# Kernel tuning notes

Hardware: AMD Instinct MI355X
Metric: run time of the kernel (lower is better)

The kernel has to match this reference:

```python
import jax, jax.numpy as jnp
import numpy as np

B, N, F_IN, F_OUT = 8, 2048, 128, 64
ALPHA = 0.2  # LeakyReLU negative slope
NEG_BIG = -9e15


def setup_inputs() -> dict:
    key = jax.random.key(0)
    k1, k2, k3, k4 = jax.random.split(key, 4)
    x = jax.random.normal(k1, (B, N, F_IN), dtype=jnp.float32)
    adj = jax.random.randint(k2, (B, N, N), 0, 2, dtype=jnp.int32)
    # xavier-uniform-ish init scale for faithfulness (gain=1.414)
    w_lim = 1.414 * np.sqrt(6.0 / (F_IN + F_OUT))
    a_lim = 1.414 * np.sqrt(6.0 / (2 * F_OUT + 1))
    weight = jax.random.uniform(k3, (F_IN, F_OUT), minval=-w_lim, maxval=w_lim, dtype=jnp.float32)
    weight2 = jax.random.uniform(k4, (2 * F_OUT, 1), minval=-a_lim, maxval=a_lim, dtype=jnp.float32)
    return {"x": x, "adj": adj, "weight": weight, "weight2": weight2}


def reference(x, adj, weight, weight2):
    # Linear projection: [B, N, F_out]
    wh = jnp.einsum("bnf,fo->bno", x, weight)
    # Additive GAT decomposition of concat-score:
    # e_ij = leakyrelu(a1 . Wh_i + a2 . Wh_j)  == original concat @ weight2
    a1 = weight2[:F_OUT, 0]   # [F_out]
    a2 = weight2[F_OUT:, 0]   # [F_out]
    s1 = wh @ a1              # [B, N]
    s2 = wh @ a2              # [B, N]
    e = s1[:, :, None] + s2[:, None, :]          # [B, N, N]
    e = jnp.where(e > 0, e, ALPHA * e)            # LeakyReLU
    e = jnp.where(adj > 0, e, NEG_BIG)            # mask non-edges
    attention = jax.nn.softmax(e, axis=2)         # [B, N, N]
    # dropout is identity in eval mode (training=False)
    out = jnp.einsum("bij,bjo->bio", attention, wh)  # [B, N, F_out]
    return jax.nn.elu(out)
```

## Files before the change

### kernel.cpp

```cpp
#include <hip/hip_runtime.h>
#include <cstdint>
#include <cstddef>

#define B_    8
#define N_    2048
#define FIN   128
#define FOUT  64
#define ALPHA 0.2f
#define NEG_BIG -9.0e15f

typedef __attribute__((ext_vector_type(8))) _Float16 half8;
typedef __attribute__((ext_vector_type(4))) float float4v;

__global__ __launch_bounds__(256, 4) void k1_wh(
    const float* __restrict__ x, const float* __restrict__ W,
    const float* __restrict__ w2, _Float16* __restrict__ whT,
    float* __restrict__ s1, float* __restrict__ s2)
{
    int t = threadIdx.x, lane = t & 63, w = t >> 6;
    float a1 = w2[lane], a2 = w2[FOUT + lane];
    int rowBase = blockIdx.x * 32 + w * 8;
    for (int rr = 0; rr < 8; ++rr) {
        int row = __builtin_amdgcn_readfirstlane(rowBase + rr);
        const float* xr = x + (size_t)row * FIN;
        float acc = 0.f;
        #pragma unroll
        for (int k = 0; k < FIN; ++k)
            acc = fmaf(xr[k], W[k * FOUT + lane], acc);
        int b = row >> 11, j = row & (N_ - 1);
        whT[((size_t)b * FOUT + lane) * N_ + j] = (_Float16)acc;
        float p1 = acc * a1, p2 = acc * a2;
        #pragma unroll
        for (int m = 32; m >= 1; m >>= 1) {
            p1 += __shfl_xor(p1, m);
            p2 += __shfl_xor(p2, m);
        }
        if (lane == 0) { s1[row] = p1; s2[row] = p2; }
    }
}

__global__ __launch_bounds__(256, 4) void k2_attn(
    const int* __restrict__ adj, const _Float16* __restrict__ whT,
    const float* __restrict__ s1, const float* __restrict__ s2,
    float* __restrict__ out)
{
    __shared__ float accL[4][16][68];
    __shared__ float lL[4][16];
    __shared__ float smaxL[4];

    int t = threadIdx.x, lane = t & 63, w = t >> 6;
    int r0 = blockIdx.x * 16;
    int b = r0 >> 11, i0 = r0 & (N_ - 1);

    const float4* s2v = (const float4*)(s2 + (size_t)b * N_);
    float4 ua = s2v[t], ub = s2v[t + 256];
    float vm = fmaxf(fmaxf(fmaxf(ua.x, ua.y), fmaxf(ua.z, ua.w)),
                     fmaxf(fmaxf(ub.x, ub.y), fmaxf(ub.z, ub.w)));
    #pragma unroll
    for (int m = 32; m >= 1; m >>= 1) vm = fmaxf(vm, __shfl_xor(vm, m));
    if (lane == 0) smaxL[w] = vm;
    __syncthreads();
    float s2max = fmaxf(fmaxf(smaxL[0], smaxL[1]), fmaxf(smaxL[2], smaxL[3]));

    int l15 = lane & 15, quad = lane >> 4;
    float s1i = s1[(size_t)b * N_ + i0 + l15];
    float mh  = s1i + s2max;
    mh = fmaxf(mh, ALPHA * mh);
    float negmh = -mh;

    float4v acc0 = {0,0,0,0}, acc1 = {0,0,0,0}, acc2 = {0,0,0,0}, acc3 = {0,0,0,0};
    float lsum = 0.f;

    const int jseg = w * 512;
    const int*      adjp = adj + ((size_t)b * N_ + i0 + l15) * N_ + jseg + quad * 8;
    const float*    s2p  = s2  + (size_t)b * N_ + jseg + quad * 8;
    const _Float16* wp   = whT + (size_t)b * FOUT * N_ + (size_t)l15 * N_ + jseg + quad * 8;

    for (int c = 0; c < 16; ++c) {
        int4   aj0 = *(const int4*)(adjp);
        int4   aj1 = *(const int4*)(adjp + 4);
        float4 sa  = *(const float4*)(s2p);
        float4 sb  = *(const float4*)(s2p + 4);
        adjp += 32; s2p += 32;

        int   aa[8] = {aj0.x, aj0.y, aj0.z, aj0.w, aj1.x, aj1.y, aj1.z, aj1.w};
        float ss[8] = {sa.x, sa.y, sa.z, sa.w, sb.x, sb.y, sb.z, sb.w};
        half8 af;
        #pragma unroll
        for (int e = 0; e < 8; ++e) {
            float v = s1i + ss[e];
            v = fmaxf(v, ALPHA * v);
            v = (aa[e] > 0) ? v : NEG_BIG;
            float tt = fmaxf(v + negmh, -76.f);
            float p = __expf(tt);
            lsum += p;
            af[e] = (_Float16)p;
        }
        half8 b0 = *(const half8*)(wp);
        half8 b1 = *(const half8*)(wp + 16 * N_);
        half8 b2 = *(const half8*)(wp + 32 * N_);
        half8 b3 = *(const half8*)(wp + 48 * N_);
        wp += 32;
        acc0 = __builtin_amdgcn_mfma_f32_16x16x32_f16(af, b0, acc0, 0, 0, 0);
        acc1 = __builtin_amdgcn_mfma_f32_16x16x32_f16(af, b1, acc1, 0, 0, 0);
        acc2 = __builtin_amdgcn_mfma_f32_16x16x32_f16(af, b2, acc2, 0, 0, 0);
        acc3 = __builtin_amdgcn_mfma_f32_16x16x32_f16(af, b3, acc3, 0, 0, 0);
    }

    lsum += __shfl_xor(lsum, 16);
    lsum += __shfl_xor(lsum, 32);

    #pragma unroll
    for (int reg = 0; reg < 4; ++reg) {
        int row = quad * 4 + reg;
        accL[w][row][ 0 + l15] = acc0[reg];
        accL[w][row][16 + l15] = acc1[reg];
        accL[w][row][32 + l15] = acc2[reg];
        accL[w][row][48 + l15] = acc3[reg];
    }
    if (quad == 0) lL[w][l15] = lsum;
    __syncthreads();

    int f = t & 63, iq = t >> 6;
    #pragma unroll
    for (int rr = 0; rr < 4; ++rr) {
        int ii = iq * 4 + rr;
        float sum = accL[0][ii][f] + accL[1][ii][f] + accL[2][ii][f] + accL[3][ii][f];
        float lt  = lL[0][ii] + lL[1][ii] + lL[2][ii] + lL[3][ii];
        float val = sum / lt;
        val = (val > 0.f) ? val : (__expf(val) - 1.f);
        out[((size_t)r0 + ii) * FOUT + f] = val;
    }
}

extern "C" void kernel_launch(void* const* d_in, const int* in_sizes, int n_in,
                              void* d_out, int out_size, void* d_ws, size_t ws_size,
                              hipStream_t stream) {
    const float* x   = (const float*)d_in[0];
    const int*   adj = (const int*)d_in[1];
    const float* W   = (const float*)d_in[2];
    const float* w2  = (const float*)d_in[3];
    float* out = (float*)d_out;

    _Float16* whT = (_Float16*)d_ws;
    float* s1 = (float*)((char*)d_ws + (size_t)B_ * FOUT * N_ * 2);
    float* s2 = s1 + (size_t)B_ * N_;

    k1_wh<<<(B_ * N_) / 32, 256, 0, stream>>>(x, W, w2, whT, s1, s2);
    k2_attn<<<(B_ * N_) / 16, 256, 0, stream>>>(adj, whT, s1, s2, out);
}
```

Before: 262.8 us.

## Split attention work by output feature via shared-memory probability tiles

Restructures the attention kernel so each wave computes softmax probabilities for 4 rows across 512 contiguous columns with coalesced adjacency loads and writes them as fp16 into a shared tile. Each wave then runs MFMA over its own 16-feature slice for all 16 rows, which removes the cross-wave reduction of four partial 16x64 accumulators. The cost is two block barriers per 512-column chunk and a shared-memory round trip for the probabilities. The exp work per element is unchanged.

```diff
diff --git a/kernel.cpp b/kernel.cpp
--- a/kernel.cpp
+++ b/kernel.cpp
@@ -44,13 +44,13 @@
     const float* __restrict__ s1, const float* __restrict__ s2,
     float* __restrict__ out)
 {
-    __shared__ float accL[4][16][68];
-    __shared__ float lL[4][16];
+    __shared__ __attribute__((aligned(16))) _Float16 pT[16][520];
+    __shared__ float lL[16];
     __shared__ float smaxL[4];
 
     int t = threadIdx.x, lane = t & 63, w = t >> 6;
-    int r0 = blockIdx.x * 16;
-    int b = r0 >> 11, i0 = r0 & (N_ - 1);
+    int b = blockIdx.x >> 7;
+    int i0 = (blockIdx.x & 127) << 4;
 
     const float4* s2v = (const float4*)(s2 + (size_t)b * N_);
     float4 ua = s2v[t], ub = s2v[t + 256];
@@ -63,73 +63,78 @@
     float s2max = fmaxf(fmaxf(smaxL[0], smaxL[1]), fmaxf(smaxL[2], smaxL[3]));
 
     int l15 = lane & 15, quad = lane >> 4;
-    float s1i = s1[(size_t)b * N_ + i0 + l15];
-    float mh  = s1i + s2max;
-    mh = fmaxf(mh, ALPHA * mh);
-    float negmh = -mh;
+    int f0 = w * 16;
 
-    float4v acc0 = {0,0,0,0}, acc1 = {0,0,0,0}, acc2 = {0,0,0,0}, acc3 = {0,0,0,0};
-    float lsum = 0.f;
-
-    const int jseg = w * 512;
-    const int*      adjp = adj + ((size_t)b * N_ + i0 + l15) * N_ + jseg + quad * 8;
-    const float*    s2p  = s2  + (size_t)b * N_ + jseg + quad * 8;
-    const _Float16* wp   = whT + (size_t)b * FOUT * N_ + (size_t)l15 * N_ + jseg + quad * 8;
-
-    for (int c = 0; c < 16; ++c) {
-        int4   aj0 = *(const int4*)(adjp);
-        int4   aj1 = *(const int4*)(adjp + 4);
-        float4 sa  = *(const float4*)(s2p);
-        float4 sb  = *(const float4*)(s2p + 4);
-        adjp += 32; s2p += 32;
-
-        int   aa[8] = {aj0.x, aj0.y, aj0.z, aj0.w, aj1.x, aj1.y, aj1.z, aj1.w};
-        float ss[8] = {sa.x, sa.y, sa.z, sa.w, sb.x, sb.y, sb.z, sb.w};
-        half8 af;
-        #pragma unroll
-        for (int e = 0; e < 8; ++e) {
-            float v = s1i + ss[e];
-            v = fmaxf(v, ALPHA * v);
-            v = (aa[e] > 0) ? v : NEG_BIG;
-            float tt = fmaxf(v + negmh, -76.f);
-            float p = __expf(tt);
-            lsum += p;
-            af[e] = (_Float16)p;
-        }
-        half8 b0 = *(const half8*)(wp);
-        half8 b1 = *(const half8*)(wp + 16 * N_);
-        half8 b2 = *(const half8*)(wp + 32 * N_);
-        half8 b3 = *(const half8*)(wp + 48 * N_);
-        wp += 32;
-        acc0 = __builtin_amdgcn_mfma_f32_16x16x32_f16(af, b0, acc0, 0, 0, 0);
-        acc1 = __builtin_amdgcn_mfma_f32_16x16x32_f16(af, b1, acc1, 0, 0, 0);
-        acc2 = __builtin_amdgcn_mfma_f32_16x16x32_f16(af, b2, acc2, 0, 0, 0);
-        acc3 = __builtin_amdgcn_mfma_f32_16x16x32_f16(af, b3, acc3, 0, 0, 0);
+    float s1r[4], negmh[4], lacc[4];
+    #pragma unroll
+    for (int rr = 0; rr < 4; ++rr) {
+        float sv = s1[(size_t)b * N_ + i0 + w * 4 + rr];
+        float mh = sv + s2max;
+        mh = fmaxf(mh, ALPHA * mh);
+        s1r[rr] = sv;
+        negmh[rr] = -mh;
+        lacc[rr] = 0.f;
     }
 
-    lsum += __shfl_xor(lsum, 16);
-    lsum += __shfl_xor(lsum, 32);
+    float4v acc = {0, 0, 0, 0};
+    const _Float16* wB = whT + ((size_t)b * FOUT + f0 + l15) * N_ + quad * 8;
+
+    for (int jc = 0; jc < N_; jc += 512) {
+        const float* s2c = s2 + (size_t)b * N_ + jc + lane * 8;
+        float4 sa = *(const float4*)s2c;
+        float4 sb = *(const float4*)(s2c + 4);
+        float ss[8] = {sa.x, sa.y, sa.z, sa.w, sb.x, sb.y, sb.z, sb.w};
+
+        #pragma unroll
+        for (int rr = 0; rr < 4; ++rr) {
+            int r = w * 4 + rr;
+            const int* ap = adj + ((size_t)b * N_ + i0 + r) * N_ + jc + lane * 8;
+            int4 aj0 = *(const int4*)ap;
+            int4 aj1 = *(const int4*)(ap + 4);
+            int aa[8] = {aj0.x, aj0.y, aj0.z, aj0.w, aj1.x, aj1.y, aj1.z, aj1.w};
+            half8 pf;
+            float ls = 0.f;
+            #pragma unroll
+            for (int e = 0; e < 8; ++e) {
+                float v = s1r[rr] + ss[e];
+                v = fmaxf(v, ALPHA * v);
+                v = (aa[e] > 0) ? v : NEG_BIG;
+                float tt = fmaxf(v + negmh[rr], -76.f);
+                float p = __expf(tt);
+                ls += p;
+                pf[e] = (_Float16)p;
+            }
+            lacc[rr] += ls;
+            *(half8*)&pT[r][lane * 8] = pf;
+        }
+
+        if (jc == N_ - 512) {
+            #pragma unroll
+            for (int rr = 0; rr < 4; ++rr) {
+                float v = lacc[rr];
+                #pragma unroll
+                for (int m = 32; m >= 1; m >>= 1) v += __shfl_xor(v, m);
+                if (lane == 0) lL[w * 4 + rr] = v;
+            }
+        }
+        __syncthreads();
+
+        const _Float16* wp = wB + jc;
+        #pragma unroll
+        for (int kk = 0; kk < 16; ++kk) {
+            half8 af = *(const half8*)&pT[l15][kk * 32 + quad * 8];
+            half8 bf = *(const half8*)(wp + kk * 32);
+            acc = __builtin_amdgcn_mfma_f32_16x16x32_f16(af, bf, acc, 0, 0, 0);
+        }
+        __syncthreads();
+    }
 
     #pragma unroll
     for (int reg = 0; reg < 4; ++reg) {
         int row = quad * 4 + reg;
-        accL[w][row][ 0 + l15] = acc0[reg];
-        accL[w][row][16 + l15] = acc1[reg];
-        accL[w][row][32 + l15] = acc2[reg];
-        accL[w][row][48 + l15] = acc3[reg];
-    }
-    if (quad == 0) lL[w][l15] = lsum;
-    __syncthreads();
-
-    int f = t & 63, iq = t >> 6;
-    #pragma unroll
-    for (int rr = 0; rr < 4; ++rr) {
-        int ii = iq * 4 + rr;
-        float sum = accL[0][ii][f] + accL[1][ii][f] + accL[2][ii][f] + accL[3][ii][f];
-        float lt  = lL[0][ii] + lL[1][ii] + lL[2][ii] + lL[3][ii];
-        float val = sum / lt;
+        float val = acc[reg] / lL[row];
         val = (val > 0.f) ? val : (__expf(val) - 1.f);
-        out[((size_t)r0 + ii) * FOUT + f] = val;
+        out[((size_t)b * N_ + i0 + row) * FOUT + f0 + l15] = val;
     }
 }
 
```

Result: faster. 254.3 us (-3.2%).
